# Performance work log

Hardware: AMD Instinct MI355X
Metric: run time of the kernel (lower is better)

The kernel has to match this reference:

```python
import jax, jax.numpy as jnp
import numpy as np

B, S, D = 2, 8192, 2048
H, HD = 16, 128
LSH_NUM_PROJS = 7
BLOCK = 256          # key/query block size for block-diagonal attention
SAMPLE = 256         # number of uniformly sampled residual columns
ROPE_BASE = 10000.0
LOG_WEIGHT = float(np.log(S / SAMPLE))  # importance weight for sampled columns


def setup_inputs() -> dict:
    key = jax.random.key(0)
    ks = jax.random.split(key, 5)
    x = jax.random.normal(ks[0], (B, S, D), jnp.float32)
    w_in = jax.random.normal(ks[1], (D, 3 * D), jnp.float32) * (D ** -0.5)
    w_out = jax.random.normal(ks[2], (D, D), jnp.float32) * (D ** -0.5)
    lsh_proj = jax.random.normal(ks[3], (HD, LSH_NUM_PROJS), jnp.float32)
    sampled_set = jax.random.randint(ks[4], (B, H, SAMPLE), 0, S, jnp.int32)
    return {"x": x, "w_in": w_in, "w_out": w_out,
            "lsh_proj": lsh_proj, "sampled_set": sampled_set}


def _rope(t):
    # t: [B, S, H, HD]; LLaMA-style half-split rotary embedding, offset=0
    half = HD // 2
    inv_freq = 1.0 / (ROPE_BASE ** (jnp.arange(half, dtype=jnp.float32) / half))
    freqs = jnp.arange(S, dtype=jnp.float32)[:, None] * inv_freq[None, :]  # [S, half]
    cos = jnp.cos(freqs)[None, :, None, :]
    sin = jnp.sin(freqs)[None, :, None, :]
    t1, t2 = t[..., :half], t[..., half:]
    return jnp.concatenate([t1 * cos - t2 * sin, t2 * cos + t1 * sin], axis=-1)


def _lse_attn(q, k, v, scale, bias=None):
    # exact attention with log-sum-exp; q [...,n,d], k/v [...,m,d]
    s = jnp.einsum('...nd,...md->...nm', q, k) * scale
    if bias is not None:
        s = s + bias
    lse = jax.nn.logsumexp(s, axis=-1, keepdims=True)   # [...,n,1]
    p = jnp.exp(s - lse)
    return jnp.einsum('...nm,...md->...nd', p, v), lse


def _hyper_attention(q, k, v, lsh_proj, sampled_set):
    # q,k,v: [B,H,S,HD]  (non-causal HyperAttention path)
    scale = HD ** -0.5

    def lsh_hash(t):
        # simhash bucket codes from sign bits of random projections
        bits = jnp.einsum('bhsd,dp->bhsp', t, lsh_proj) > 0
        powers = (2 ** jnp.arange(LSH_NUM_PROJS)).astype(jnp.int32)
        return jnp.sum(bits.astype(jnp.int32) * powers, axis=-1)  # [B,H,S]

    q_idx = jnp.argsort(lsh_hash(q), axis=-1, stable=True)
    k_idx = jnp.argsort(lsh_hash(k), axis=-1, stable=True)
    q_idx_inv = jnp.argsort(q_idx, axis=-1, stable=True)
    gather = lambda t, i: jnp.take_along_axis(t, i[..., None], axis=2)

    qs = gather(q, q_idx)
    ks_ = gather(k, k_idx)
    vs = gather(v, k_idx)

    # 1. block-diagonal exact attention on LSH-sorted order
    nb = S // BLOCK
    qb = qs.reshape(B, H, nb, BLOCK, HD)
    kb = ks_.reshape(B, H, nb, BLOCK, HD)
    vb = vs.reshape(B, H, nb, BLOCK, HD)
    attn_blk, lse_blk = _lse_attn(qb, kb, vb, scale)
    attn_blk = attn_blk.reshape(B, H, S, HD)
    lse_blk = lse_blk.reshape(B, H, S, 1)

    # 2. residual: uniformly sampled columns (indices into sorted key order),
    #    masking columns already covered by the query's diagonal block
    k_sub = gather(ks_, sampled_set)   # [B,H,m,HD]
    v_sub = gather(vs, sampled_set)
    q_block_id = jnp.arange(S, dtype=jnp.int32) // BLOCK          # [S]
    s_block_id = sampled_set // BLOCK                             # [B,H,m]
    neg = jnp.finfo(q.dtype).min
    bias = jnp.where(q_block_id[None, None, :, None] == s_block_id[:, :, None, :],
                     neg, jnp.array(0.0, q.dtype))                # [B,H,S,m]
    attn_res, lse_res = _lse_attn(qs, k_sub, v_sub, scale, bias=bias)
    lse_res = lse_res + LOG_WEIGHT

    # 3. merge the two partial softmax results (online-softmax combine)
    lse = jnp.logaddexp(lse_blk, lse_res)
    attn = attn_blk * jnp.exp(lse_blk - lse) + attn_res * jnp.exp(lse_res - lse)

    # undo query sort
    return gather(attn, q_idx_inv)


def reference(x, w_in, w_out, lsh_proj, sampled_set):
    qkv = x @ w_in                           # [B,S,3D]
    q, k, v = jnp.split(qkv, 3, axis=-1)
    r4 = lambda t: t.reshape(B, S, H, HD)
    q, k, v = _rope(r4(q)), _rope(r4(k)), r4(v)
    tr = lambda t: t.transpose(0, 2, 1, 3)   # -> [B,H,S,HD]
    out = _hyper_attention(tr(q), tr(k), tr(v), lsh_proj, sampled_set)
    out = out.transpose(0, 2, 1, 3).reshape(B, S, D)
    return out @ w_out
```

## Files before the change

kernel.cpp:

```cpp
#include <hip/hip_runtime.h>
#include <stdint.h>

typedef _Float16 f16;
typedef _Float16 f16x8 __attribute__((ext_vector_type(8)));
typedef float f32x4 __attribute__((ext_vector_type(4)));
typedef uint32_t u32;

#define SEQ 8192
#define NH 16
#define HDIM 128
#define BHCNT 32
#define KDIM 2048
#define SCALE 0.08838834764831845f
#define LOGW 3.4657359027997265f
#define TAU1 0.06f
#define TAU 6e-3f
#define MAXWL 32768
#define BCAP 1024

__device__ __forceinline__ f32x4 mfma16(f16x8 a, f16x8 b, f32x4 c){
  return __builtin_amdgcn_mfma_f32_16x16x32_f16(a, b, c, 0, 0, 0);
}

__device__ __forceinline__ void g2l16(const f16* g, f16* l){
  __builtin_amdgcn_global_load_lds(
      (const __attribute__((address_space(1))) void*)g,
      (__attribute__((address_space(3))) void*)l, 16, 0, 0);
}

__global__ __launch_bounds__(256) void split_x_k(const float* __restrict__ x,
                                                 f16* __restrict__ xh){
  size_t i = ((size_t)blockIdx.x * 256 + threadIdx.x) * 4;
  float4 v = *(const float4*)(x + i);
  union { f16 h[4]; ushort4 u; } a;
  a.h[0]=(f16)v.x; a.h[1]=(f16)v.y; a.h[2]=(f16)v.z; a.h[3]=(f16)v.w;
  *(ushort4*)(xh + i) = a.u;
}

__global__ void transpose_k(const float* __restrict__ in, f16* __restrict__ ohi,
                            f16* __restrict__ olo, int Kd, int Nd, int NLO){
  __shared__ float t[32][33];
  int tx = threadIdx.x, ty = threadIdx.y;
  int n0 = blockIdx.x*32, k0 = blockIdx.y*32;
  #pragma unroll
  for (int i=0;i<4;i++) t[ty+i*8][tx] = in[(size_t)(k0+ty+i*8)*Nd + n0+tx];
  __syncthreads();
  #pragma unroll
  for (int i=0;i<4;i++){
    int n = n0 + ty + i*8, k = k0 + tx;
    float v = t[tx][ty+i*8];
    f16 h = (f16)v;
    ohi[(size_t)n*Kd + k] = h;
    if (n < NLO) olo[(size_t)n*Kd + k] = (f16)(v - (float)h);
  }
}

__global__ __launch_bounds__(256) void rope_table_k(float* __restrict__ ct, float* __restrict__ st){
  int i = blockIdx.x * 256 + threadIdx.x;
  int s = i >> 6, d = i & 63;
  float p32 = (float)pow(10000.0, (double)d / 64.0);
  float inv = __fdiv_rn(1.0f, p32);
  float f = __fmul_rn((float)s, inv);
  double a = (double)f;
  ct[i] = (float)cos(a);
  st[i] = (float)sin(a);
}

__global__ void zero_k(int* p){ p[0] = 0; p[1] = 0; p[2] = 0; }

__global__ void diag_k(const int* __restrict__ flags, float* __restrict__ out){
  int c = flags[0];
  if (c == 0 || c >= MAXWL || flags[2]) out[0] = 1.0e9f + (float)c;
}

template<int MODE, int NC, int GS>
__global__ __launch_bounds__(256) void gemm_k(
    const f16* __restrict__ A, const f16* __restrict__ Bt,
    f16* __restrict__ q16, f16* __restrict__ k16, f16* __restrict__ v16,
    float* __restrict__ o0, int N){
  __shared__ f16 sm[8192];
  const int tid = threadIdx.x, lane = tid & 63, wave = tid >> 6;
  const int wr = wave >> 1, wc = wave & 1;
  const int wg = blockIdx.x;
  const int xcd = wg & 7, wgl = wg >> 3;
  const int grp = wgl / (16*GS);
  const int rem = wgl % (16*GS);
  const int brow = xcd*16 + rem / GS;
  const int bcol = grp*GS + rem % GS;
  const int g = lane >> 4, q_ = lane & 15;
  f32x4 acc[4][4];
  #pragma unroll
  for (int m=0;m<4;m++)
    #pragma unroll
    for (int n=0;n<4;n++) acc[m][n] = (f32x4){0.f,0.f,0.f,0.f};
  const int srow = tid >> 2, sseg = tid & 3;
  const int scol = (sseg ^ (srow & 3)) * 8;
  const f16* ga0 = A  + (size_t)(brow*128 + srow)*KDIM + scol;
  const f16* gb0 = Bt + (size_t)(bcol*128 + srow)*KDIM + scol;
  f16* As = sm; f16* Bs = sm + 4096;
  f16* dA0 = As + wave*512; f16* dA1 = As + 2048 + wave*512;
  f16* dB0 = Bs + wave*512; f16* dB1 = Bs + 2048 + wave*512;
  const int aoff = (wr*64 + q_)*32 + (g ^ (q_ & 3))*8;
  const int boff = (wc*64 + q_)*32 + (g ^ (q_ & 3))*8;
  for (int kt = 0; kt < KDIM/32; ++kt){
    const size_t ko = (size_t)kt * 32;
    g2l16(ga0 + ko, dA0); g2l16(ga0 + (size_t)64*KDIM + ko, dA1);
    g2l16(gb0 + ko, dB0); g2l16(gb0 + (size_t)64*KDIM + ko, dB1);
    __syncthreads();
    f16x8 af[4];
    #pragma unroll
    for (int m=0;m<4;m++) af[m] = *(const f16x8*)&As[aoff + m*16*32];
    #pragma unroll
    for (int n=0;n<4;n++){
      f16x8 bf = *(const f16x8*)&Bs[boff + n*16*32];
      #pragma unroll
      for (int m=0;m<4;m++) acc[m][n] = mfma16(af[m], bf, acc[m][n]);
    }
    __syncthreads();
  }
  #pragma unroll
  for (int m=0;m<4;m++)
    #pragma unroll
    for (int n=0;n<4;n++)
      #pragma unroll
      for (int j=0;j<4;j++){
        int row = brow*128 + wr*64 + m*16 + g*4 + j;
        int col = bcol*128 + wc*64 + n*16 + q_;
        float v = acc[m][n][j];
        if constexpr (MODE == 0){
          o0[(size_t)row * N + col] = v;
        } else {
          int b = row >> 13, s = row & 8191;
          int sec = col >> 11;
          int cl = col & 2047;
          int h = cl >> 7, hd = cl & 127;
          f16* dst = (sec == 0) ? q16 : ((sec == 1) ? k16 : v16);
          dst[(((size_t)b*NH + h)*SEQ + s)*HDIM + hd] = (f16)v;
        }
      }
}

__global__ __launch_bounds__(256) void rope_hash_k(f16* __restrict__ qk, const float* __restrict__ ct,
    const float* __restrict__ st, const float* __restrict__ proj, int* __restrict__ hout,
    int tag, int* __restrict__ wl, int* __restrict__ wcnt){
  const int lane = threadIdx.x & 63, wave = threadIdx.x >> 6;
  const int s = blockIdx.x * 4 + wave, bh = blockIdx.y;
  f16* row = qk + ((size_t)bh * SEQ + s) * HDIM;
  float vx = (float)row[2*lane], vy = (float)row[2*lane+1];
  float ox = __shfl_xor(vx, 32), oy = __shfl_xor(vy, 32);
  const int dl = 2*lane, di = dl & 63;
  const float* cb = ct + (size_t)s*64; const float* sb = st + (size_t)s*64;
  float c0 = cb[di], c1 = cb[di+1], sn0 = sb[di], sn1 = sb[di+1];
  float r0, r1;
  if (lane < 32){ r0 = vx*c0 - ox*sn0; r1 = vy*c1 - oy*sn1; }
  else          { r0 = vx*c0 + ox*sn0; r1 = vy*c1 + oy*sn1; }
  union { f16 h[2]; u32 u; } pk;
  pk.h[0] = (f16)r0; pk.h[1] = (f16)r1;
  *(u32*)(row + dl) = pk.u;
  float part[7];
  #pragma unroll
  for (int p=0;p<7;p++) part[p] = r0*proj[dl*7+p] + r1*proj[(dl+1)*7+p];
  #pragma unroll
  for (int off=32; off>=1; off>>=1){
    #pragma unroll
    for (int p=0;p<7;p++) part[p] += __shfl_xor(part[p], off);
  }
  if (lane == 0){
    int hs = 0; float mn = 1e30f;
    #pragma unroll
    for (int p=0;p<7;p++){ if (part[p] > 0.f) hs |= (1<<p); mn = fminf(mn, fabsf(part[p])); }
    hout[bh*SEQ + s] = hs;
    if (mn < TAU1){
      int w = atomicAdd(wcnt, 1);
      if (w < MAXWL){ wl[2*w] = (bh<<1) | tag; wl[2*w+1] = s; }
    }
  }
}

__global__ __launch_bounds__(256) void bucket_k(const int* __restrict__ wl, const int* __restrict__ wcnt,
    int* __restrict__ wl2, int* __restrict__ cnt2, int* __restrict__ flags){
  const int bucket = blockIdx.x;
  __shared__ int lcnt;
  if (threadIdx.x == 0) lcnt = 0;
  __syncthreads();
  int count = wcnt[0]; if (count > MAXWL) count = MAXWL;
  for (int i = threadIdx.x; i < count; i += 256){
    int tagbh = wl[2*i];
    int tag = tagbh & 1, h = (tagbh >> 1) & 15;
    if (tag*16 + h == bucket){
      int pos = atomicAdd(&lcnt, 1);
      if (pos < BCAP) wl2[bucket*BCAP + pos] = (tagbh << 13) | wl[2*i+1];
    }
  }
  __syncthreads();
  if (threadIdx.x == 0){
    cnt2[bucket] = (lcnt > BCAP) ? BCAP : lcnt;
    if (lcnt > BCAP) atomicExch(&flags[2], 1);
  }
}

__global__ __launch_bounds__(256) void t2_k(const float* __restrict__ x,
    const f16* __restrict__ wh, const f16* __restrict__ wlo,
    const int* __restrict__ wl2, const int* __restrict__ cnt2,
    const float* __restrict__ ct, const float* __restrict__ st, const float* __restrict__ proj,
    int* __restrict__ hq, int* __restrict__ hk, int* __restrict__ wl3, int* __restrict__ wcnt3){
  const int bucket = blockIdx.y;
  const int nrows = cnt2[bucket];
  const int base = blockIdx.x * 64;
  if (base >= nrows) return;
  const int tid = threadIdx.x, lane = tid & 63, wave = tid >> 6;
  const int g = lane >> 4, q_ = lane & 15;
  __shared__ f16 Ah[64*32], Alo[64*32], Bh[128*32], Bl[128*32];
  __shared__ float S[64][128];
  __shared__ int rs[64], ent[64];
  if (tid < 64){
    int idx = base + tid;
    int e = wl2[bucket*BCAP + (idx < nrows ? idx : 0)];
    ent[tid] = e;
    int s = e & 8191;
    int b = e >> 18;
    rs[tid] = b * SEQ + s;
  }
  __syncthreads();
  const int tag = bucket >> 4, h = bucket & 15;
  const f16* Wh = wh  + ((size_t)(tag*2048 + h*128)) * KDIM;
  const f16* Wl = wlo + ((size_t)(tag*2048 + h*128)) * KDIM;
  f32x4 acc[8];
  #pragma unroll
  for (int n=0;n<8;n++) acc[n] = (f32x4){0.f,0.f,0.f,0.f};
  const int arow = tid >> 2, aseg = tid & 3;
  const int bcol = tid >> 1, bhalf = tid & 1;
  const size_t abase = (size_t)rs[arow]*KDIM + aseg*8;
  const size_t bbase = (size_t)bcol*KDIM + bhalf*16;
  for (int kt = 0; kt < 64; ++kt){
    const int k0 = kt*32;
    {
      union { float4 f4[2]; float f[8]; } xa;
      xa.f4[0] = *(const float4*)(x + abase + k0);
      xa.f4[1] = *(const float4*)(x + abase + k0 + 4);
      union { f16 h[8]; f16x8 v; } hh, ll;
      #pragma unroll
      for (int i=0;i<8;i++){
        f16 hv = (f16)xa.f[i];
        hh.h[i] = hv;
        ll.h[i] = (f16)(xa.f[i] - (float)hv);
      }
      *(f16x8*)&Ah [arow*32 + aseg*8] = hh.v;
      *(f16x8*)&Alo[arow*32 + aseg*8] = ll.v;
    }
    *(f16x8*)&Bh[bcol*32 + bhalf*16]     = *(const f16x8*)(Wh + bbase + k0);
    *(f16x8*)&Bh[bcol*32 + bhalf*16 + 8] = *(const f16x8*)(Wh + bbase + k0 + 8);
    *(f16x8*)&Bl[bcol*32 + bhalf*16]     = *(const f16x8*)(Wl + bbase + k0);
    *(f16x8*)&Bl[bcol*32 + bhalf*16 + 8] = *(const f16x8*)(Wl + bbase + k0 + 8);
    __syncthreads();
    f16x8 ah = *(const f16x8*)&Ah [(wave*16 + q_)*32 + g*8];
    f16x8 al = *(const f16x8*)&Alo[(wave*16 + q_)*32 + g*8];
    #pragma unroll
    for (int n=0;n<8;n++){
      f16x8 bh8 = *(const f16x8*)&Bh[(n*16 + q_)*32 + g*8];
      f16x8 bl8 = *(const f16x8*)&Bl[(n*16 + q_)*32 + g*8];
      acc[n] = mfma16(ah, bh8, acc[n]);
      acc[n] = mfma16(ah, bl8, acc[n]);
      acc[n] = mfma16(al, bh8, acc[n]);
    }
    __syncthreads();
  }
  #pragma unroll
  for (int n=0;n<8;n++)
    #pragma unroll
    for (int j=0;j<4;j++)
      S[wave*16 + g*4 + j][n*16 + q_] = acc[n][j];
  __syncthreads();
  for (int r = 0; r < 16; ++r){
    int row = wave*16 + r;
    int gidx = base + row;
    if (gidx >= nrows) break;
    int e = ent[row];
    int s = e & 8191;
    int tagbh = e >> 13;
    int bh = tagbh >> 1;
    float vx = S[row][2*lane], vy = S[row][2*lane+1];
    float ox = __shfl_xor(vx, 32), oy = __shfl_xor(vy, 32);
    const int dl = 2*lane, di = dl & 63;
    float c0 = ct[(size_t)s*64 + di], c1v = ct[(size_t)s*64 + di + 1];
    float sn0 = st[(size_t)s*64 + di], sn1 = st[(size_t)s*64 + di + 1];
    float r0, r1;
    if (lane < 32){ r0 = vx*c0 - ox*sn0; r1 = vy*c1v - oy*sn1; }
    else          { r0 = vx*c0 + ox*sn0; r1 = vy*c1v + oy*sn1; }
    float part[7];
    #pragma unroll
    for (int p=0;p<7;p++) part[p] = r0*proj[dl*7+p] + r1*proj[(dl+1)*7+p];
    #pragma unroll
    for (int off=32; off>=1; off>>=1){
      #pragma unroll
      for (int p=0;p<7;p++) part[p] += __shfl_xor(part[p], off);
    }
    if (lane == 0){
      int hs = 0; float mn = 1e30f;
      #pragma unroll
      for (int p=0;p<7;p++){ if (part[p] > 0.f) hs |= (1<<p); mn = fminf(mn, fabsf(part[p])); }
      ((tagbh & 1) ? hk : hq)[bh*SEQ + s] = hs;
      if (mn < TAU){
        int w = atomicAdd(wcnt3, 1);
        if (w < MAXWL){ wl3[2*w] = tagbh; wl3[2*w+1] = s; }
      }
    }
  }
}

__global__ __launch_bounds__(256) void fixup_k(const float* __restrict__ x, const float* __restrict__ w_in,
    const float* __restrict__ proj, const float* __restrict__ ct, const float* __restrict__ st,
    const int* __restrict__ wl, const int* __restrict__ wcnt,
    int* __restrict__ hq, int* __restrict__ hk){
  const int lane = threadIdx.x & 63, wave = threadIdx.x >> 6;
  const int gw = blockIdx.x * 4 + wave, nw = gridDim.x * 4;
  int count = *wcnt; if (count > MAXWL) count = MAXWL;
  for (int e = gw; e < count; e += nw){
    int tagbh = wl[2*e], s = wl[2*e+1];
    int tag = tagbh & 1, bh = tagbh >> 1;
    int b = bh >> 4, h = bh & 15;
    const float* xr = x + ((size_t)b*SEQ + s)*KDIM;
    const int c0i = tag*2048 + h*128 + lane;
    double a0 = 0.0, a1 = 0.0;
    for (int j = 0; j < KDIM; ++j){
      double xv = (double)xr[j];
      a0 += xv * (double)w_in[(size_t)j*6144 + c0i];
      a1 += xv * (double)w_in[(size_t)j*6144 + c0i + 64];
    }
    double c = (double)ct[(size_t)s*64 + lane];
    double sn = (double)st[(size_t)s*64 + lane];
    double r0 = a0*c - a1*sn;
    double r1 = a1*c + a0*sn;
    int hs = 0;
    #pragma unroll
    for (int p = 0; p < 7; ++p){
      double part = r0 * (double)proj[lane*7+p] + r1 * (double)proj[(lane+64)*7+p];
      #pragma unroll
      for (int off = 32; off >= 1; off >>= 1) part += __shfl_xor(part, off);
      if (part > 0.0) hs |= (1<<p);
    }
    if (lane == 0) (tag ? hk : hq)[bh*SEQ + s] = hs;
  }
}

__global__ __launch_bounds__(256) void sort_k(const int* __restrict__ hsh, int* __restrict__ idx){
  const int bh = blockIdx.x, tid = threadIdx.x;
  __shared__ unsigned char hl[SEQ];
  __shared__ unsigned short hist[128*256];
  __shared__ unsigned int part[256];
  const int* hrow = hsh + bh*SEQ;
  for (int i = tid; i < SEQ; i += 256) hl[i] = (unsigned char)hrow[i];
  u32* h32 = (u32*)hist;
  for (int i = tid; i < 128*256/2; i += 256) h32[i] = 0;
  __syncthreads();
  #pragma unroll 1
  for (int j = 0; j < 32; ++j){
    int hv = hl[tid*32 + j];
    hist[hv*256 + tid] = (unsigned short)(hist[hv*256 + tid] + 1);
  }
  __syncthreads();
  unsigned int s = 0;
  #pragma unroll 1
  for (int f = tid*128; f < tid*128 + 128; ++f) s += hist[f];
  part[tid] = s;
  __syncthreads();
  for (int off = 1; off < 256; off <<= 1){
    unsigned int v = (tid >= off) ? part[tid - off] : 0u;
    __syncthreads();
    part[tid] += v;
    __syncthreads();
  }
  unsigned int run = (tid == 0) ? 0u : part[tid - 1];
  #pragma unroll 1
  for (int f = tid*128; f < tid*128 + 128; ++f){
    unsigned short c = hist[f];
    hist[f] = (unsigned short)run;
    run += c;
  }
  __syncthreads();
  int* orow = idx + bh*SEQ;
  #pragma unroll 1
  for (int j = 0; j < 32; ++j){
    int i = tid*32 + j;
    int hv = hl[i];
    unsigned short p = hist[hv*256 + tid];
    hist[hv*256 + tid] = (unsigned short)(p + 1);
    orow[p] = i;
  }
}

__global__ __launch_bounds__(512) void attn_k(const f16* __restrict__ qr, const f16* __restrict__ kr,
    const f16* __restrict__ v, const int* __restrict__ qidx, const int* __restrict__ kidx,
    const int* __restrict__ smp, f16* __restrict__ out){
  const int tid = threadIdx.x, lane = tid & 63, wave = tid >> 6;
  const int blk = blockIdx.x, bh = blockIdx.y;
  const int b = bh >> 4, h = bh & 15;
  const int qblock = blk >> 1;
  __shared__ f16 Kl[32*136];
  __shared__ f16 Vt[128*40];
  __shared__ float biasl[256];
  __shared__ int kid[512];
  const int g = lane >> 4, q_ = lane & 15;
  {
    int j = tid;
    int kpos;
    if (j < 256) kpos = qblock*256 + j;
    else {
      kpos = smp[bh*256 + (j-256)];
      biasl[j-256] = ((kpos >> 8) == qblock) ? -1e30f : LOGW;
    }
    kid[j] = kidx[bh*SEQ + kpos];
  }
  const int qpos = blk*128 + wave*16 + q_;
  const int qi = qidx[bh*SEQ + qpos];
  const f16* qb = qr + ((size_t)bh*SEQ + qi)*HDIM;
  f16x8 qf[4];
  #pragma unroll
  for (int c=0;c<4;c++) qf[c] = *(const f16x8*)(qb + c*32 + g*8);
  f32x4 O[8];
  #pragma unroll
  for (int c=0;c<8;c++) O[c] = (f32x4){0.f,0.f,0.f,0.f};
  float m_run = -1e30f, l_run = 0.f;
  __syncthreads();
  const int kkK = tid >> 3, segK = tid & 7;
  const int kk2 = tid & 15, d0 = (tid >> 4) * 8;
  f16x8 pk0, pk1, pv0, pv1;
  if (tid < 256){
    int krw = kid[kkK];
    const f16* ks = kr + ((size_t)bh*SEQ + krw)*HDIM + segK*16;
    pk0 = *(const f16x8*)ks; pk1 = *(const f16x8*)(ks + 8);
    int r0 = kid[2*kk2], r1 = kid[2*kk2 + 1];
    pv0 = *(const f16x8*)(v + ((size_t)bh*SEQ + r0)*HDIM + d0);
    pv1 = *(const f16x8*)(v + ((size_t)bh*SEQ + r1)*HDIM + d0);
  }
  for (int t = 0; t < 16; ++t){
    if (tid < 256){
      *(f16x8*)&Kl[kkK*136 + segK*16]     = pk0;
      *(f16x8*)&Kl[kkK*136 + segK*16 + 8] = pk1;
      #pragma unroll
      for (int i=0;i<8;i++){
        union { f16 h[2]; u32 u; } pr;
        pr.h[0] = pv0[i]; pr.h[1] = pv1[i];
        *(u32*)&Vt[(d0+i)*40 + 2*kk2] = pr.u;
      }
    }
    __syncthreads();
    if (t < 15 && tid < 256){
      int jb = (t+1)*32;
      int krw = kid[jb + kkK];
      const f16* ks = kr + ((size_t)bh*SEQ + krw)*HDIM + segK*16;
      pk0 = *(const f16x8*)ks; pk1 = *(const f16x8*)(ks + 8);
      int r0 = kid[jb + 2*kk2], r1 = kid[jb + 2*kk2 + 1];
      pv0 = *(const f16x8*)(v + ((size_t)bh*SEQ + r0)*HDIM + d0);
      pv1 = *(const f16x8*)(v + ((size_t)bh*SEQ + r1)*HDIM + d0);
    }
    f32x4 c0 = (f32x4){0.f,0.f,0.f,0.f}, c1 = (f32x4){0.f,0.f,0.f,0.f};
    #pragma unroll
    for (int c=0;c<4;c++){
      f16x8 k0 = *(const f16x8*)&Kl[q_*136 + c*32 + g*8];
      f16x8 k1 = *(const f16x8*)&Kl[(16+q_)*136 + c*32 + g*8];
      c0 = mfma16(k0, qf[c], c0);
      c1 = mfma16(k1, qf[c], c1);
    }
    float sc[8];
    if (t < 8){
      #pragma unroll
      for (int j=0;j<4;j++){ sc[j] = c0[j]*SCALE; sc[4+j] = c1[j]*SCALE; }
    } else {
      const float* bb = &biasl[(t-8)*32];
      #pragma unroll
      for (int j=0;j<4;j++){ sc[j] = c0[j]*SCALE + bb[g*4+j]; sc[4+j] = c1[j]*SCALE + bb[16+g*4+j]; }
    }
    float mx = sc[0];
    #pragma unroll
    for (int i=1;i<8;i++) mx = fmaxf(mx, sc[i]);
    mx = fmaxf(mx, __shfl_xor(mx, 16));
    mx = fmaxf(mx, __shfl_xor(mx, 32));
    float mnew = fmaxf(m_run, mx);
    float al = __expf(m_run - mnew);
    float p[8]; float ps = 0.f;
    #pragma unroll
    for (int i=0;i<8;i++){ p[i] = __expf(sc[i] - mnew); ps += p[i]; }
    ps += __shfl_xor(ps, 16);
    ps += __shfl_xor(ps, 32);
    l_run = l_run * al + ps;
    m_run = mnew;
    float aj0 = __shfl(al, g*4+0), aj1 = __shfl(al, g*4+1);
    float aj2 = __shfl(al, g*4+2), aj3 = __shfl(al, g*4+3);
    #pragma unroll
    for (int c=0;c<8;c++){ O[c][0]*=aj0; O[c][1]*=aj1; O[c][2]*=aj2; O[c][3]*=aj3; }
    union { f16 h[2]; u32 u; } pk;
    pk.h[0]=(f16)p[0]; pk.h[1]=(f16)p[1]; u32 A0 = pk.u;
    pk.h[0]=(f16)p[2]; pk.h[1]=(f16)p[3]; u32 A1 = pk.u;
    pk.h[0]=(f16)p[4]; pk.h[1]=(f16)p[5]; u32 B0 = pk.u;
    pk.h[0]=(f16)p[6]; pk.h[1]=(f16)p[7]; u32 B1 = pk.u;
    int srcA = (((2*g)&3)<<4) | q_;
    int srcB = ((((2*g)+1)&3)<<4) | q_;
    bool selh = g >= 2;
    u32 xa0 = __shfl(A0, srcA), xb0 = __shfl(B0, srcA);
    u32 xa1 = __shfl(A1, srcA), xb1 = __shfl(B1, srcA);
    u32 xa2 = __shfl(A0, srcB), xb2 = __shfl(B0, srcB);
    u32 xa3 = __shfl(A1, srcB), xb3 = __shfl(B1, srcB);
    union { u32 w[4]; f16x8 f; } pf;
    pf.w[0] = selh ? xb0 : xa0;
    pf.w[1] = selh ? xb1 : xa1;
    pf.w[2] = selh ? xb2 : xa2;
    pf.w[3] = selh ? xb3 : xa3;
    #pragma unroll
    for (int c=0;c<8;c++){
      f16x8 vf = *(const f16x8*)&Vt[(c*16 + q_)*40 + g*8];
      O[c] = mfma16(pf.f, vf, O[c]);
    }
    __syncthreads();
  }
  float li0 = 1.f/__shfl(l_run, g*4+0), li1 = 1.f/__shfl(l_run, g*4+1);
  float li2 = 1.f/__shfl(l_run, g*4+2), li3 = 1.f/__shfl(l_run, g*4+3);
  const int posbase = blk*128 + wave*16;
  #pragma unroll
  for (int j=0;j<4;j++){
    float li = (j==0)?li0:((j==1)?li1:((j==2)?li2:li3));
    int sorig = qidx[bh*SEQ + posbase + g*4 + j];
    f16* dst = out + (((size_t)b*SEQ + sorig)*NH + h)*HDIM;
    #pragma unroll
    for (int c=0;c<8;c++) dst[c*16 + q_] = (f16)(O[c][j] * li);
  }
}

extern "C" void kernel_launch(void* const* d_in, const int* in_sizes, int n_in,
                              void* d_out, int out_size, void* d_ws, size_t ws_size,
                              hipStream_t stream) {
  (void)in_sizes; (void)n_in; (void)out_size; (void)ws_size;
  const float* x     = (const float*)d_in[0];
  const float* w_in  = (const float*)d_in[1];
  const float* w_out = (const float*)d_in[2];
  const float* proj  = (const float*)d_in[3];
  const int*   smp   = (const int*)d_in[4];
  float* out = (float*)d_out;

  char* ws = (char*)d_ws;
  size_t off = 0;
  auto alloc = [&](size_t bytes){ void* p = ws + off; off += (bytes + 255) & ~(size_t)255; return p; };
  f16*   xh   = (f16*)alloc((size_t)16384*2048*2);
  f16*   wh   = (f16*)alloc((size_t)6144*2048*2);
  f16*   wl   = (f16*)alloc((size_t)4096*2048*2);
  f16*   wo   = (f16*)alloc((size_t)2048*2048*2);
  f16*   qf   = (f16*)alloc((size_t)BHCNT*SEQ*HDIM*2);
  f16*   kf   = (f16*)alloc((size_t)BHCNT*SEQ*HDIM*2);
  f16*   vv   = (f16*)alloc((size_t)BHCNT*SEQ*HDIM*2);
  f16*   attn = (f16*)alloc((size_t)BHCNT*SEQ*HDIM*2);
  float* cost = (float*)alloc((size_t)SEQ*64*4);
  float* sint = (float*)alloc((size_t)SEQ*64*4);
  int*   hq   = (int*)alloc((size_t)BHCNT*SEQ*4);
  int*   hk   = (int*)alloc((size_t)BHCNT*SEQ*4);
  int*   qidx = (int*)alloc((size_t)BHCNT*SEQ*4);
  int*   kidx = (int*)alloc((size_t)BHCNT*SEQ*4);
  int*   wlst = (int*)alloc((size_t)MAXWL*2*4);
  int*   wlst2= (int*)alloc((size_t)32*BCAP*4);
  int*   wlst3= (int*)alloc((size_t)MAXWL*2*4);
  int*   cnt2 = (int*)alloc(256);
  int*   flags= (int*)alloc(256);

  int* wcnt  = flags;
  int* wcnt3 = flags + 1;

  zero_k<<<1, 1, 0, stream>>>(flags);
  split_x_k<<<32768, 256, 0, stream>>>(x, xh);
  transpose_k<<<dim3(192,64), dim3(32,8), 0, stream>>>(w_in, wh, wl, 2048, 6144, 4096);
  transpose_k<<<dim3(64,64),  dim3(32,8), 0, stream>>>(w_out, wo, nullptr, 2048, 2048, 0);
  rope_table_k<<<2048, 256, 0, stream>>>(cost, sint);

  gemm_k<1,48,6><<<6144, 256, 0, stream>>>(xh, wh, qf, kf, vv, nullptr, 0);

  rope_hash_k<<<dim3(2048,32), 256, 0, stream>>>(qf, cost, sint, proj, hq, 0, wlst, wcnt);
  rope_hash_k<<<dim3(2048,32), 256, 0, stream>>>(kf, cost, sint, proj, hk, 1, wlst, wcnt);

  bucket_k<<<32, 256, 0, stream>>>(wlst, wcnt, wlst2, cnt2, flags);
  t2_k<<<dim3(16,32), 256, 0, stream>>>(x, wh, wl, wlst2, cnt2, cost, sint, proj,
                                        hq, hk, wlst3, wcnt3);
  fixup_k<<<512, 256, 0, stream>>>(x, w_in, proj, cost, sint, wlst3, wcnt3, hq, hk);

  sort_k<<<32, 256, 0, stream>>>(hq, qidx);
  sort_k<<<32, 256, 0, stream>>>(hk, kidx);

  attn_k<<<dim3(64,32), 512, 0, stream>>>(qf, kf, vv, qidx, kidx, smp, attn);

  gemm_k<0,16,8><<<2048, 256, 0, stream>>>(attn, wo, nullptr, nullptr, nullptr, out, 2048);

  diag_k<<<1, 1, 0, stream>>>(flags, out);
}
```

Before: 1.614 ms.

## Bucket fp64 fixup work by head/tag and split accumulation chains

Adds a second bucketing pass that groups the near-boundary hash fixup rows by (tag, head). The fp64 fixup kernel then runs one block per bucket, so rows in a block share the same w_in columns and get better cache reuse. The inner fp64 dot product now uses four independent accumulators to break the serial dependency chain. The grid shrinks from 512 blocks to 32, which lowers parallelism, and buckets with more rows than the smaller cap are truncated (the overflow flag is set).

```diff
diff --git a/kernel.cpp b/kernel.cpp
--- a/kernel.cpp
+++ b/kernel.cpp
@@ -17,6 +17,7 @@
 #define TAU 6e-3f
 #define MAXWL 32768
 #define BCAP 1024
+#define BCAP3 512
 
 __device__ __forceinline__ f32x4 mfma16(f16x8 a, f16x8 b, f32x4 c){
   return __builtin_amdgcn_mfma_f32_16x16x32_f16(a, b, c, 0, 0, 0);
@@ -177,6 +178,7 @@
   }
 }
 
+template<int CAP>
 __global__ __launch_bounds__(256) void bucket_k(const int* __restrict__ wl, const int* __restrict__ wcnt,
     int* __restrict__ wl2, int* __restrict__ cnt2, int* __restrict__ flags){
   const int bucket = blockIdx.x;
@@ -189,13 +191,13 @@
     int tag = tagbh & 1, h = (tagbh >> 1) & 15;
     if (tag*16 + h == bucket){
       int pos = atomicAdd(&lcnt, 1);
-      if (pos < BCAP) wl2[bucket*BCAP + pos] = (tagbh << 13) | wl[2*i+1];
+      if (pos < CAP) wl2[bucket*CAP + pos] = (tagbh << 13) | wl[2*i+1];
     }
   }
   __syncthreads();
   if (threadIdx.x == 0){
-    cnt2[bucket] = (lcnt > BCAP) ? BCAP : lcnt;
-    if (lcnt > BCAP) atomicExch(&flags[2], 1);
+    cnt2[bucket] = (lcnt > CAP) ? CAP : lcnt;
+    if (lcnt > CAP) atomicExch(&flags[2], 1);
   }
 }
 
@@ -310,23 +312,30 @@
 
 __global__ __launch_bounds__(256) void fixup_k(const float* __restrict__ x, const float* __restrict__ w_in,
     const float* __restrict__ proj, const float* __restrict__ ct, const float* __restrict__ st,
-    const int* __restrict__ wl, const int* __restrict__ wcnt,
+    const int* __restrict__ wl4, const int* __restrict__ cnt4,
     int* __restrict__ hq, int* __restrict__ hk){
+  const int bucket = blockIdx.x;
+  const int n = cnt4[bucket];
   const int lane = threadIdx.x & 63, wave = threadIdx.x >> 6;
-  const int gw = blockIdx.x * 4 + wave, nw = gridDim.x * 4;
-  int count = *wcnt; if (count > MAXWL) count = MAXWL;
-  for (int e = gw; e < count; e += nw){
-    int tagbh = wl[2*e], s = wl[2*e+1];
+  for (int e = wave; e < n; e += 4){
+    int entry = wl4[bucket*BCAP3 + e];
+    int s = entry & 8191;
+    int tagbh = entry >> 13;
     int tag = tagbh & 1, bh = tagbh >> 1;
     int b = bh >> 4, h = bh & 15;
     const float* xr = x + ((size_t)b*SEQ + s)*KDIM;
     const int c0i = tag*2048 + h*128 + lane;
-    double a0 = 0.0, a1 = 0.0;
-    for (int j = 0; j < KDIM; ++j){
-      double xv = (double)xr[j];
-      a0 += xv * (double)w_in[(size_t)j*6144 + c0i];
-      a1 += xv * (double)w_in[(size_t)j*6144 + c0i + 64];
-    }
+    double a0c[4] = {0,0,0,0}, a1c[4] = {0,0,0,0};
+    for (int j = 0; j < KDIM; j += 4){
+      #pragma unroll
+      for (int u2 = 0; u2 < 4; ++u2){
+        double xv = (double)xr[j + u2];
+        a0c[u2] += xv * (double)w_in[(size_t)(j + u2)*6144 + c0i];
+        a1c[u2] += xv * (double)w_in[(size_t)(j + u2)*6144 + c0i + 64];
+      }
+    }
+    double a0 = (a0c[0] + a0c[1]) + (a0c[2] + a0c[3]);
+    double a1 = (a1c[0] + a1c[1]) + (a1c[2] + a1c[3]);
     double c = (double)ct[(size_t)s*64 + lane];
     double sn = (double)st[(size_t)s*64 + lane];
     double r0 = a0*c - a1*sn;
@@ -557,7 +566,9 @@
   int*   wlst = (int*)alloc((size_t)MAXWL*2*4);
   int*   wlst2= (int*)alloc((size_t)32*BCAP*4);
   int*   wlst3= (int*)alloc((size_t)MAXWL*2*4);
+  int*   wlst4= (int*)alloc((size_t)32*BCAP3*4);
   int*   cnt2 = (int*)alloc(256);
+  int*   cnt4 = (int*)alloc(256);
   int*   flags= (int*)alloc(256);
 
   int* wcnt  = flags;
@@ -574,10 +585,11 @@
   rope_hash_k<<<dim3(2048,32), 256, 0, stream>>>(qf, cost, sint, proj, hq, 0, wlst, wcnt);
   rope_hash_k<<<dim3(2048,32), 256, 0, stream>>>(kf, cost, sint, proj, hk, 1, wlst, wcnt);
 
-  bucket_k<<<32, 256, 0, stream>>>(wlst, wcnt, wlst2, cnt2, flags);
+  bucket_k<BCAP><<<32, 256, 0, stream>>>(wlst, wcnt, wlst2, cnt2, flags);
   t2_k<<<dim3(16,32), 256, 0, stream>>>(x, wh, wl, wlst2, cnt2, cost, sint, proj,
                                         hq, hk, wlst3, wcnt3);
-  fixup_k<<<512, 256, 0, stream>>>(x, w_in, proj, cost, sint, wlst3, wcnt3, hq, hk);
+  bucket_k<BCAP3><<<32, 256, 0, stream>>>(wlst3, wcnt3, wlst4, cnt4, flags);
+  fixup_k<<<32, 256, 0, stream>>>(x, w_in, proj, cost, sint, wlst4, cnt4, hq, hk);
 
   sort_k<<<32, 256, 0, stream>>>(hq, qidx);
   sort_k<<<32, 256, 0, stream>>>(hk, kidx);
```

After: 4.153 ms. 2.57x slower.
